# Optimization experiments

Measured on AMD Instinct MI355X. Metric: run time of the kernel, lower is better.

## Reference

```python
import jax, jax.numpy as jnp
import numpy as np

B, T, D = 512, 256, 256
U = 512  # lstm_units


def setup_inputs() -> dict:
    key = jax.random.key(0)
    ks = jax.random.split(key, 8)
    s_in = 1.0 / np.sqrt(D)
    s_h = 1.0 / np.sqrt(U)
    return {
        "x": jax.random.normal(ks[0], (B, T, D), dtype=jnp.float32),
        "Wx": jax.random.normal(ks[1], (D, 4 * U), dtype=jnp.float32) * s_in,
        "Wh": jax.random.normal(ks[2], (U, 4 * U), dtype=jnp.float32) * s_h,
        "b": jax.random.normal(ks[3], (4 * U,), dtype=jnp.float32) * 0.01,
        "W1": jax.random.normal(ks[4], (U, 128), dtype=jnp.float32) * s_h,
        "b1": jnp.zeros((128,), dtype=jnp.float32),
        "W2": jax.random.normal(ks[5], (128, 10), dtype=jnp.float32) * (1.0 / np.sqrt(128)),
        "b2": jnp.zeros((10,), dtype=jnp.float32),
    }


def _lstm_last_hidden(x, Wx, Wh, b):
    # Precompute input projections for all timesteps: [B,T,4U] -> scan axis T
    xz = jnp.einsum("btd,dg->tbg", x, Wx) + b  # [T,B,4U]

    def step(carry, xz_t):
        h, c = carry
        z = xz_t + h @ Wh  # [B,4U]
        i, f, g, o = jnp.split(z, 4, axis=-1)  # keras gate order: i,f,c,o
        i = jax.nn.sigmoid(i)
        f = jax.nn.sigmoid(f)
        g = jnp.tanh(g)
        o = jax.nn.sigmoid(o)
        c = f * c + i * g
        h = o * jnp.tanh(c)
        return (h, c), None

    h0 = jnp.zeros((x.shape[0], Wh.shape[0]), dtype=x.dtype)
    (h, _), _ = jax.lax.scan(step, (h0, h0), xz)
    return h  # last hidden state [B,U]


def reference(x, Wx, Wh, b, W1, b1, W2, b2):
    h = _lstm_last_hidden(x, Wx, Wh, b)
    h = jax.nn.relu(h @ W1 + b1)
    return jax.nn.softmax(h @ W2 + b2, axis=-1)
```

## Files before the change

### kernel.cpp

```cpp
#include <hip/hip_runtime.h>

#define B_SZ 512
#define T_SZ 256
#define D_SZ 256
#define U_SZ 512

typedef float  f32x4  __attribute__((ext_vector_type(4)));
typedef short  short8 __attribute__((ext_vector_type(8)));
typedef __bf16 bf16x8 __attribute__((ext_vector_type(8)));

static __device__ __forceinline__ unsigned short f2bf(float f) {
  unsigned u = __builtin_bit_cast(unsigned, f);
  return (unsigned short)((u + 0x7FFFu + ((u >> 16) & 1u)) >> 16);
}

static __device__ __forceinline__ f32x4 mfma_bf16(short8 a, short8 b, f32x4 c) {
  return __builtin_amdgcn_mfma_f32_16x16x32_bf16(
      __builtin_bit_cast(bf16x8, a), __builtin_bit_cast(bf16x8, b), c, 0, 0, 0);
}

static __device__ __forceinline__ float sigm(float x) {
  return 1.f / (1.f + __expf(-x));
}
static __device__ __forceinline__ float tanh_fast(float x) {
  return 1.f - 2.f / (__expf(2.f * x) + 1.f);
}

__global__ __launch_bounds__(256) void wt_kernel(const float* __restrict__ Wx,
                                                 const float* __restrict__ Wh,
                                                 unsigned short* __restrict__ Wt) {
  __shared__ float tile[32][33];
  const int ct = blockIdx.x;
  const int kt = blockIdx.y;
  const int tx = threadIdx.x & 31;
  const int ty = threadIdx.x >> 5;
  const int k0 = kt * 32;
#pragma unroll
  for (int q = 0; q < 4; ++q) {
    int kl = ty + q * 8;
    int kg = k0 + kl;
    float v = (kg < 256) ? Wx[(size_t)kg * 2048 + ct * 32 + tx]
                         : Wh[(size_t)(kg - 256) * 2048 + ct * 32 + tx];
    tile[kl][tx] = v;
  }
  __syncthreads();
#pragma unroll
  for (int q = 0; q < 4; ++q) {
    int cl = ty + q * 8;
    Wt[(size_t)(ct * 32 + cl) * 768 + k0 + tx] = f2bf(tile[tx][cl]);
  }
}

__global__ __launch_bounds__(256, 1) void lstm_kernel(
    const float* __restrict__ x, const unsigned short* __restrict__ Wt,
    const float* __restrict__ bias, unsigned short* __restrict__ hbuf,
    unsigned* __restrict__ cnt, float* __restrict__ hfin) {
  extern __shared__ char smem[];
  const int tid  = threadIdx.x;
  const int lane = tid & 63;
  const int wv   = tid >> 6;
  const int mt   = wv & 1;
  const int uh   = wv >> 1;
  const int g    = blockIdx.x & 15;
  const int s    = blockIdx.x >> 4;
  const int col  = lane & 15;
  const int kgrp = lane >> 4;
  const int ug   = s * 32 + uh * 16 + col;

  short8 Bfr[96];
#pragma unroll
  for (int kt = 0; kt < 24; ++kt) {
#pragma unroll
    for (int gg = 0; gg < 4; ++gg) {
      const unsigned short* p =
          Wt + (size_t)(gg * 512 + ug) * 768 + kgrp * 8 + kt * 32;
      Bfr[kt * 4 + gg] = *(const short8*)p;
    }
  }
  float bias_g[4];
#pragma unroll
  for (int gg = 0; gg < 4; ++gg) bias_g[gg] = bias[gg * 512 + ug];

  f32x4 cst = {0.f, 0.f, 0.f, 0.f};
  int p = 0;
  for (int t = 0; t < 256; ++t) {
    if (t > 0) {
      if (tid == 0) {
        const unsigned* cp = cnt + (g << 8) + (t - 1);
        while (__hip_atomic_load(cp, __ATOMIC_RELAXED,
                                 __HIP_MEMORY_SCOPE_AGENT) < 16u) {
        }
      }
      __syncthreads();
    }

#pragma unroll
    for (int i = 0; i < 4; ++i) {
      int ch = tid + i * 256;
      int row = ch >> 5;
      int k0 = (ch & 31) * 8;
      const float* xp = x + ((size_t)(g * 32 + row) * T_SZ + t) * D_SZ + k0;
      float4 a  = *(const float4*)xp;
      float4 b2 = *(const float4*)(xp + 4);
      short8 v;
      v[0] = (short)f2bf(a.x);  v[1] = (short)f2bf(a.y);
      v[2] = (short)f2bf(a.z);  v[3] = (short)f2bf(a.w);
      v[4] = (short)f2bf(b2.x); v[5] = (short)f2bf(b2.y);
      v[6] = (short)f2bf(b2.z); v[7] = (short)f2bf(b2.w);
      unsigned byte = ((unsigned)(row * 1536 + k0 * 2)) ^ ((row & 7) << 4);
      *(short8*)(smem + byte) = v;
    }
    const unsigned short* hr =
        hbuf + ((size_t)p << 18) + ((size_t)(g * 32) << 9);
#pragma unroll
    for (int i = 0; i < 16; ++i) {
      int ch = tid + i * 256;
      int row = ch >> 7;
      int c4 = ch & 127;
      const unsigned long long* hp =
          (const unsigned long long*)(hr + ((size_t)row << 9) + c4 * 4);
      unsigned long long v = __hip_atomic_load(hp, __ATOMIC_RELAXED,
                                               __HIP_MEMORY_SCOPE_AGENT);
      unsigned byte =
          ((unsigned)(row * 1536 + (256 + c4 * 4) * 2)) ^ ((row & 7) << 4);
      *(unsigned long long*)(smem + byte) = v;
    }
    __syncthreads();

    f32x4 acc[4];
#pragma unroll
    for (int gg = 0; gg < 4; ++gg) acc[gg] = (f32x4){0.f, 0.f, 0.f, 0.f};
    const int arow = mt * 16 + col;
#pragma unroll
    for (int kt = 0; kt < 24; ++kt) {
      unsigned byte = ((unsigned)(arow * 1536 + (kgrp * 8 + kt * 32) * 2)) ^
                      ((arow & 7) << 4);
      short8 af = *(const short8*)(smem + byte);
      acc[0] = mfma_bf16(af, Bfr[kt * 4 + 0], acc[0]);
      acc[1] = mfma_bf16(af, Bfr[kt * 4 + 1], acc[1]);
      acc[2] = mfma_bf16(af, Bfr[kt * 4 + 2], acc[2]);
      acc[3] = mfma_bf16(af, Bfr[kt * 4 + 3], acc[3]);
    }

#pragma unroll
    for (int j = 0; j < 4; ++j) {
      float zi = acc[0][j] + bias_g[0];
      float zf = acc[1][j] + bias_g[1];
      float zg = acc[2][j] + bias_g[2];
      float zo = acc[3][j] + bias_g[3];
      float ii = sigm(zi);
      float ff = sigm(zf);
      float gv = tanh_fast(zg);
      float oo = sigm(zo);
      float cv = ff * cst[j] + ii * gv;
      cst[j] = cv;
      float hv = oo * tanh_fast(cv);
      int brow = g * 32 + mt * 16 + kgrp * 4 + j;
      if (t == 255) {
        hfin[(size_t)brow * 512 + ug] = hv;
      } else {
        unsigned short* hp =
            hbuf + (((size_t)(p ^ 1)) << 18) + ((size_t)brow << 9) + ug;
        __hip_atomic_store(hp, f2bf(hv), __ATOMIC_RELAXED,
                           __HIP_MEMORY_SCOPE_AGENT);
      }
    }

    if (t == 255) break;

    __syncthreads();
    if (tid == 0) {
      __hip_atomic_fetch_add(cnt + (g << 8) + t, 1u, __ATOMIC_RELAXED,
                             __HIP_MEMORY_SCOPE_AGENT);
    }
    p ^= 1;
  }
}

__global__ __launch_bounds__(128) void mlp_kernel(
    const float* __restrict__ hfin, const float* __restrict__ W1,
    const float* __restrict__ b1, const float* __restrict__ W2,
    const float* __restrict__ b2, float* __restrict__ out) {
  __shared__ float hrow[512];
  __shared__ float act[128];
  __shared__ float lg[10];
  const int b = blockIdx.x;
  const int tid = threadIdx.x;
#pragma unroll
  for (int i = 0; i < 4; ++i)
    hrow[tid + i * 128] = hfin[(size_t)b * 512 + tid + i * 128];
  __syncthreads();
  float s = b1[tid];
#pragma unroll 8
  for (int k = 0; k < 512; ++k) s += hrow[k] * W1[(size_t)k * 128 + tid];
  act[tid] = fmaxf(s, 0.f);
  __syncthreads();
  if (tid < 10) {
    float l = b2[tid];
#pragma unroll 8
    for (int k = 0; k < 128; ++k) l += act[k] * W2[(size_t)k * 10 + tid];
    lg[tid] = l;
  }
  __syncthreads();
  if (tid == 0) {
    float m = lg[0];
    for (int j = 1; j < 10; ++j) m = fmaxf(m, lg[j]);
    float e[10];
    float sum = 0.f;
    for (int j = 0; j < 10; ++j) {
      e[j] = expf(lg[j] - m);
      sum += e[j];
    }
    float inv = 1.f / sum;
    for (int j = 0; j < 10; ++j) out[(size_t)b * 10 + j] = e[j] * inv;
  }
}

extern "C" void kernel_launch(void* const* d_in, const int* in_sizes, int n_in,
                              void* d_out, int out_size, void* d_ws,
                              size_t ws_size, hipStream_t stream) {
  const float* x    = (const float*)d_in[0];
  const float* Wx   = (const float*)d_in[1];
  const float* Wh   = (const float*)d_in[2];
  const float* bias = (const float*)d_in[3];
  const float* W1   = (const float*)d_in[4];
  const float* b1   = (const float*)d_in[5];
  const float* W2   = (const float*)d_in[6];
  const float* b2   = (const float*)d_in[7];
  float* out = (float*)d_out;

  char* ws = (char*)d_ws;
  unsigned short* hbuf = (unsigned short*)ws;
  unsigned* cnt        = (unsigned*)(ws + 1048576);
  unsigned short* Wt   = (unsigned short*)(ws + 2097152);
  float* hfin          = (float*)(ws + 2097152 + 3145728);

  hipMemsetAsync(d_ws, 0, 1048576 + 16384, stream);

  wt_kernel<<<dim3(64, 24), 256, 0, stream>>>(Wx, Wh, Wt);

  hipFuncSetAttribute((const void*)lstm_kernel,
                      hipFuncAttributeMaxDynamicSharedMemorySize, 49152);
  lstm_kernel<<<256, 256, 49152, stream>>>(x, Wt, bias, hbuf, cnt, hfin);

  mlp_kernel<<<512, 128, 0, stream>>>(hfin, W1, b1, W2, b2, out);
}
```

Baseline: 2.644 ms.

## Prefetch next-step x into double-buffered LDS and use per-block ready flags

The x tile for step t+1 is loaded into registers before the cross-block wait and converted into a double-buffered LDS region during the current step, moving global x loads off the critical recurrence path. The shared atomic counter is replaced by per-producer flag words that 16 lanes of every wave poll directly, which removes the post-spin block barrier and the atomic-add contention. LDS usage grows to 64 KB, the flag region grows, and register pressure rises from holding the prefetched x values.

```diff
diff --git a/kernel.cpp b/kernel.cpp
--- a/kernel.cpp
+++ b/kernel.cpp
@@ -54,7 +54,7 @@
 __global__ __launch_bounds__(256, 1) void lstm_kernel(
     const float* __restrict__ x, const unsigned short* __restrict__ Wt,
     const float* __restrict__ bias, unsigned short* __restrict__ hbuf,
-    unsigned* __restrict__ cnt, float* __restrict__ hfin) {
+    unsigned* __restrict__ flags, float* __restrict__ hfin) {
   extern __shared__ char smem[];
   const int tid  = threadIdx.x;
   const int lane = tid & 63;
@@ -81,35 +81,51 @@
 #pragma unroll
   for (int gg = 0; gg < 4; ++gg) bias_g[gg] = bias[gg * 512 + ug];
 
+#pragma unroll
+  for (int i = 0; i < 4; ++i) {
+    int ch = tid + i * 256;
+    int row = ch >> 5;
+    int k0 = (ch & 31) * 8;
+    const float* xp = x + ((size_t)(g * 32 + row) * T_SZ + 0) * D_SZ + k0;
+    float4 a  = *(const float4*)xp;
+    float4 b2 = *(const float4*)(xp + 4);
+    short8 v;
+    v[0] = (short)f2bf(a.x);  v[1] = (short)f2bf(a.y);
+    v[2] = (short)f2bf(a.z);  v[3] = (short)f2bf(a.w);
+    v[4] = (short)f2bf(b2.x); v[5] = (short)f2bf(b2.y);
+    v[6] = (short)f2bf(b2.z); v[7] = (short)f2bf(b2.w);
+    unsigned byte = ((unsigned)(row * 512 + k0 * 2)) ^ ((row & 7) << 4);
+    *(short8*)(smem + byte) = v;
+  }
+
   f32x4 cst = {0.f, 0.f, 0.f, 0.f};
   int p = 0;
+  int par = 0;
   for (int t = 0; t < 256; ++t) {
+    float4 xa[4], xb[4];
+    if (t < 255) {
+#pragma unroll
+      for (int i = 0; i < 4; ++i) {
+        int ch = tid + i * 256;
+        int row = ch >> 5;
+        int k0 = (ch & 31) * 8;
+        const float* xp =
+            x + ((size_t)(g * 32 + row) * T_SZ + (t + 1)) * D_SZ + k0;
+        xa[i] = *(const float4*)xp;
+        xb[i] = *(const float4*)(xp + 4);
+      }
+    }
+
     if (t > 0) {
-      if (tid == 0) {
-        const unsigned* cp = cnt + (g << 8) + (t - 1);
-        while (__hip_atomic_load(cp, __ATOMIC_RELAXED,
-                                 __HIP_MEMORY_SCOPE_AGENT) < 16u) {
+      const unsigned* fb = flags + (((unsigned)(g << 8) + (t - 1)) << 4);
+      if (lane < 16) {
+        while (__hip_atomic_load(fb + lane, __ATOMIC_RELAXED,
+                                 __HIP_MEMORY_SCOPE_AGENT) == 0u) {
         }
       }
-      __syncthreads();
-    }
-
-#pragma unroll
-    for (int i = 0; i < 4; ++i) {
-      int ch = tid + i * 256;
-      int row = ch >> 5;
-      int k0 = (ch & 31) * 8;
-      const float* xp = x + ((size_t)(g * 32 + row) * T_SZ + t) * D_SZ + k0;
-      float4 a  = *(const float4*)xp;
-      float4 b2 = *(const float4*)(xp + 4);
-      short8 v;
-      v[0] = (short)f2bf(a.x);  v[1] = (short)f2bf(a.y);
-      v[2] = (short)f2bf(a.z);  v[3] = (short)f2bf(a.w);
-      v[4] = (short)f2bf(b2.x); v[5] = (short)f2bf(b2.y);
-      v[6] = (short)f2bf(b2.z); v[7] = (short)f2bf(b2.w);
-      unsigned byte = ((unsigned)(row * 1536 + k0 * 2)) ^ ((row & 7) << 4);
-      *(short8*)(smem + byte) = v;
-    }
+      __builtin_amdgcn_sched_barrier(0);
+    }
+
     const unsigned short* hr =
         hbuf + ((size_t)p << 18) + ((size_t)(g * 32) << 9);
 #pragma unroll
@@ -122,19 +138,41 @@
       unsigned long long v = __hip_atomic_load(hp, __ATOMIC_RELAXED,
                                                __HIP_MEMORY_SCOPE_AGENT);
       unsigned byte =
-          ((unsigned)(row * 1536 + (256 + c4 * 4) * 2)) ^ ((row & 7) << 4);
+          (32768u + (unsigned)(row * 1024 + c4 * 8)) ^ ((row & 7) << 4);
       *(unsigned long long*)(smem + byte) = v;
     }
     __syncthreads();
+
+    if (t < 255) {
+#pragma unroll
+      for (int i = 0; i < 4; ++i) {
+        int ch = tid + i * 256;
+        int row = ch >> 5;
+        int k0 = (ch & 31) * 8;
+        short8 v;
+        v[0] = (short)f2bf(xa[i].x);  v[1] = (short)f2bf(xa[i].y);
+        v[2] = (short)f2bf(xa[i].z);  v[3] = (short)f2bf(xa[i].w);
+        v[4] = (short)f2bf(xb[i].x);  v[5] = (short)f2bf(xb[i].y);
+        v[6] = (short)f2bf(xb[i].z);  v[7] = (short)f2bf(xb[i].w);
+        unsigned byte = ((unsigned)((par ^ 1) * 16384 + row * 512 + k0 * 2)) ^
+                        ((row & 7) << 4);
+        *(short8*)(smem + byte) = v;
+      }
+    }
 
     f32x4 acc[4];
 #pragma unroll
     for (int gg = 0; gg < 4; ++gg) acc[gg] = (f32x4){0.f, 0.f, 0.f, 0.f};
     const int arow = mt * 16 + col;
+    const unsigned rsw = (unsigned)((arow & 7) << 4);
 #pragma unroll
     for (int kt = 0; kt < 24; ++kt) {
-      unsigned byte = ((unsigned)(arow * 1536 + (kgrp * 8 + kt * 32) * 2)) ^
-                      ((arow & 7) << 4);
+      unsigned byte;
+      if (kt < 8)
+        byte = ((unsigned)(par * 16384 + arow * 512 + kt * 64 + kgrp * 16)) ^ rsw;
+      else
+        byte = (32768u +
+                (unsigned)(arow * 1024 + (kt - 8) * 64 + kgrp * 16)) ^ rsw;
       short8 af = *(const short8*)(smem + byte);
       acc[0] = mfma_bf16(af, Bfr[kt * 4 + 0], acc[0]);
       acc[1] = mfma_bf16(af, Bfr[kt * 4 + 1], acc[1]);
@@ -170,10 +208,11 @@
 
     __syncthreads();
     if (tid == 0) {
-      __hip_atomic_fetch_add(cnt + (g << 8) + t, 1u, __ATOMIC_RELAXED,
-                             __HIP_MEMORY_SCOPE_AGENT);
+      __hip_atomic_store(flags + ((((unsigned)(g << 8) + t) << 4) + s), 1u,
+                         __ATOMIC_RELAXED, __HIP_MEMORY_SCOPE_AGENT);
     }
     p ^= 1;
+    par ^= 1;
   }
 }
 
@@ -231,17 +270,17 @@
 
   char* ws = (char*)d_ws;
   unsigned short* hbuf = (unsigned short*)ws;
-  unsigned* cnt        = (unsigned*)(ws + 1048576);
+  unsigned* flags      = (unsigned*)(ws + 1048576);
   unsigned short* Wt   = (unsigned short*)(ws + 2097152);
   float* hfin          = (float*)(ws + 2097152 + 3145728);
 
-  hipMemsetAsync(d_ws, 0, 1048576 + 16384, stream);
+  hipMemsetAsync(d_ws, 0, 1048576 + 262144, stream);
 
   wt_kernel<<<dim3(64, 24), 256, 0, stream>>>(Wx, Wh, Wt);
 
   hipFuncSetAttribute((const void*)lstm_kernel,
-                      hipFuncAttributeMaxDynamicSharedMemorySize, 49152);
-  lstm_kernel<<<256, 256, 49152, stream>>>(x, Wt, bias, hbuf, cnt, hfin);
+                      hipFuncAttributeMaxDynamicSharedMemorySize, 65536);
+  lstm_kernel<<<256, 256, 65536, stream>>>(x, Wt, bias, hbuf, flags, hfin);
 
   mlp_kernel<<<512, 128, 0, stream>>>(hfin, W1, b1, W2, b2, out);
 }
```

New measurement: 2.832 ms. 1.07x slower.
